# Kernel optimization log

Measured on AMD Instinct MI355X. Metric: run time of the kernel, lower is better.

Reference implementation:

```python
import jax, jax.numpy as jnp
import numpy as np

S, B, L, D, H, NOP = 4, 8, 512, 128, 128, 64  # segments, batch, seg_len, input_dim, hidden, n_operators
W = S * L  # 2048 total words
FT = 0.1   # forget-gate floor


def _norm_mat(m):
    # divide each row by its count of nonzero entries (torch normalize_matrix)
    cnt = (m != 0).sum(-1, keepdims=True).astype(m.dtype)
    return m / (cnt + 1e-30)


def _l2(x):
    return x / (jnp.linalg.norm(x, axis=-1, keepdims=True) + 1e-30)


def setup_inputs() -> dict:
    key = jax.random.key(0)
    ks = jax.random.split(key, 16)
    word_outputs = jax.random.normal(ks[0], (S, B, L, D), jnp.float32)
    node_hidden = jax.random.normal(ks[1], (B, D), jnp.float32)
    op_embedding = jax.random.normal(ks[2], (B, NOP, D), jnp.float32)
    word_operator = (jax.random.uniform(ks[3], (B, W, NOP)) < 0.05).astype(jnp.float32)
    word_word = (jax.random.uniform(ks[4], (B, W, W)) < 0.02).astype(jnp.float32)
    depend_relation = (jax.random.uniform(ks[5], (S, B, L, L)) < 0.05).astype(jnp.float32)
    word_exist_matrix = (jax.random.uniform(ks[6], (B, W, W)) < 0.9).astype(jnp.float32)
    word_exist_sequence = (jax.random.uniform(ks[7], (B, W)) < 0.9).astype(jnp.float32)
    goal_word = (jax.random.uniform(ks[8], (B, W)) < 0.2).astype(jnp.float32)

    def lin(k, fi, fo):
        k1, k2 = jax.random.split(k)
        s = 1.0 / np.sqrt(fi).astype(np.float32)
        return (jax.random.uniform(k1, (fi, fo), jnp.float32, -s, s),
                jax.random.uniform(k2, (fo,), jnp.float32, -s, s))

    o_w_W, o_w_b = lin(ks[9], D, H)
    wk_W, wk_b = lin(ks[10], D, H)
    ws_W, ws_b = lin(ks[11], D, H)
    up_W, up_b = lin(ks[12], 3 * H, D)
    wg_W, wg_b = lin(ks[13], D, D)
    fg_W, fg_b = lin(ks[14], 2 * D, D)
    return dict(word_outputs=word_outputs, node_hidden=node_hidden, op_embedding=op_embedding,
                word_operator=word_operator, word_word=word_word, depend_relation=depend_relation,
                word_exist_matrix=word_exist_matrix, word_exist_sequence=word_exist_sequence,
                goal_word=goal_word, o_w_W=o_w_W, o_w_b=o_w_b, wk_W=wk_W, wk_b=wk_b,
                ws_W=ws_W, ws_b=ws_b, up_W=up_W, up_b=up_b, wg_W=wg_W, wg_b=wg_b,
                fg_W=fg_W, fg_b=fg_b)


def reference(word_outputs, node_hidden, op_embedding, word_operator, word_word,
              depend_relation, word_exist_matrix, word_exist_sequence, goal_word,
              o_w_W, o_w_b, wk_W, wk_b, ws_W, ws_b, up_W, up_b, wg_W, wg_b, fg_W, fg_b):
    # cat(word_outputs, dim=1) -> [B, W, D]
    all_word = word_outputs.transpose(1, 0, 2, 3).reshape(B, W, D)
    # operator aggregation: [B,W,NOP] @ o_w(op_embedding) -> [B,W,H], L2-normalized
    word_o = _l2(jnp.einsum('bwo,boh->bwh', word_operator, op_embedding @ o_w_W + o_w_b))
    # knowledge aggregation over masked word-word adjacency
    adj_k = _norm_mat(word_word * word_exist_matrix)
    word_w_k = _l2(jnp.einsum('bvw,bwh->bvh', adj_k, all_word @ wk_W + wk_b))
    # per-segment dependency aggregation, then concat along word dim
    seg = jnp.einsum('sbij,sbjh->sbih', _norm_mat(depend_relation), word_outputs @ ws_W + ws_b)
    word_w_s = _l2(seg.transpose(1, 0, 2, 3).reshape(B, W, H))
    neighbor = jnp.concatenate([word_o, word_w_k, word_w_s], axis=-1)  # [B, W, 3H]
    word_updated = jax.nn.relu(neighbor @ up_W + up_b)  # [B, W, D]
    # goal pooling: bmm([B,1,W],[B,W,D]) -> [B,D]
    gw = _norm_mat(goal_word * word_exist_sequence)
    goal_w = jnp.einsum('bw,bwd->bd', gw, word_updated)
    goal_updated = jax.nn.relu(goal_w @ wg_W + wg_b)
    forget = jax.nn.sigmoid(jnp.concatenate([goal_w, node_hidden], axis=-1) @ fg_W + fg_b)
    return jnp.maximum(forget, FT) * node_hidden + (1.0 - forget) * goal_updated
```

## Files before the change

kernel.cpp:

```cpp
#include <hip/hip_runtime.h>
#include <math.h>

#define Sn 4
#define Bn 8
#define Ln 512
#define Dn 128
#define Hn 128
#define NOPn 64
#define Wn 2048


__device__ __forceinline__ float bf2f(unsigned short u) {
    return __uint_as_float(((unsigned int)u) << 16);
}
__device__ __forceinline__ float bflo(unsigned int u) {
    return __uint_as_float(u << 16);
}
__device__ __forceinline__ float bfhi(unsigned int u) {
    return __uint_as_float(u & 0xFFFF0000u);
}
__device__ __forceinline__ unsigned short f2bf(float f) {
    unsigned int u = __float_as_uint(f);
    return (unsigned short)((u + 0x7FFFu + ((u >> 16) & 1u)) >> 16);
}

typedef __attribute__((ext_vector_type(8))) short bf16x8;
typedef __attribute__((ext_vector_type(4))) float f32x4;

__global__ __launch_bounds__(256) void prep_k(const float* __restrict__ A,
                                              const float* __restrict__ W1,
                                              const float* __restrict__ W2,
                                              const float* __restrict__ b1,
                                              const float* __restrict__ b2,
                                              unsigned short* __restrict__ C1,
                                              unsigned short* __restrict__ C2,
                                              const float* __restrict__ ope,
                                              const float* __restrict__ owW,
                                              const float* __restrict__ owb,
                                              unsigned short* __restrict__ oph,
                                              const float* __restrict__ goal,
                                              const float* __restrict__ wes,
                                              int* __restrict__ widx,
                                              int* __restrict__ wcnt,
                                              float* __restrict__ gwacc,
                                              const float* __restrict__ upW,
                                              unsigned short* __restrict__ upWbf) {
    __shared__ __align__(16) unsigned char smem[33792];
    const int bid = blockIdx.x, tid = threadIdx.x;

    if (bid < 264) {
        unsigned short (*WT)[132] = reinterpret_cast<unsigned short(*)[132]>(smem);
        const bool dual = bid < 256;
        const int m0 = dual ? bid * 64 : (bid - 256) * 64;
        const float* Asrc = dual ? A : ope;
        const int lane = tid & 63, wr = tid >> 6;
        const int rloc = lane & 15, bsel = lane >> 4;

        bf16x8 af[4];
        const float* Arow = Asrc + (size_t)(m0 + wr * 16 + rloc) * 128;
#pragma unroll
        for (int ks = 0; ks < 4; ++ks) {
            float4 a0 = *reinterpret_cast<const float4*>(Arow + ks * 32 + 4 * bsel);
            float4 a1 = *reinterpret_cast<const float4*>(Arow + ks * 32 + 16 + 4 * bsel);
            af[ks][0] = (short)f2bf(a0.x); af[ks][1] = (short)f2bf(a0.y);
            af[ks][2] = (short)f2bf(a0.z); af[ks][3] = (short)f2bf(a0.w);
            af[ks][4] = (short)f2bf(a1.x); af[ks][5] = (short)f2bf(a1.y);
            af[ks][6] = (short)f2bf(a1.z); af[ks][7] = (short)f2bf(a1.w);
        }

        const int nmat = dual ? 2 : 1;
        for (int mat = 0; mat < nmat; ++mat) {
            const float* Wsrc = dual ? (mat ? W2 : W1) : owW;
            const float* bias = dual ? (mat ? b2 : b1) : owb;
            unsigned short* Cdst = dual ? (mat ? C2 : C1) : oph;
            __syncthreads();
            for (int idx = tid * 4; idx < 128 * 128; idx += 1024) {
                const int k = idx >> 7, c = idx & 127;
                float4 v = *reinterpret_cast<const float4*>(Wsrc + (size_t)k * 128 + c);
                WT[c + 0][k] = f2bf(v.x);
                WT[c + 1][k] = f2bf(v.y);
                WT[c + 2][k] = f2bf(v.z);
                WT[c + 3][k] = f2bf(v.w);
            }
            __syncthreads();

            f32x4 acc[8];
#pragma unroll
            for (int tl = 0; tl < 8; ++tl) acc[tl] = (f32x4){0.f, 0.f, 0.f, 0.f};
#pragma unroll
            for (int ks = 0; ks < 4; ++ks) {
#pragma unroll
                for (int tl = 0; tl < 8; ++tl) {
                    const unsigned short* p = &WT[tl * 16 + rloc][ks * 32 + 4 * bsel];
                    bf16x8 bfv;
#pragma unroll
                    for (int j = 0; j < 4; ++j) {
                        bfv[j]     = (short)p[j];
                        bfv[4 + j] = (short)p[16 + j];
                    }
                    acc[tl] = __builtin_amdgcn_mfma_f32_16x16x32_bf16(
                        af[ks], bfv, acc[tl], 0, 0, 0);
                }
            }
#pragma unroll
            for (int tl = 0; tl < 8; ++tl) {
                const int col = tl * 16 + rloc;
                const float bv = bias[col];
#pragma unroll
                for (int q = 0; q < 4; ++q) {
                    const int row = m0 + wr * 16 + bsel * 4 + q;
                    Cdst[(size_t)row * 128 + col] = f2bf(acc[tl][q] + bv);
                }
            }
        }
    } else if (bid < 272) {
        int* cnt = reinterpret_cast<int*>(smem);
        const int b = bid - 264;
        if (tid == 0) *cnt = 0;
        __syncthreads();
#pragma unroll
        for (int j = 0; j < 8; ++j) {
            const int w = tid * 8 + j;
            if (goal[b * Wn + w] != 0.f && wes[b * Wn + w] != 0.f) {
                const int p = atomicAdd(cnt, 1);
                if (p < 512) widx[b * 512 + p] = w;
            }
        }
        __syncthreads();
        if (tid == 0) wcnt[b] = *cnt < 512 ? *cnt : 512;
    } else if (bid == 272) {
        for (int idx = tid; idx < 1024; idx += 256) gwacc[idx] = 0.f;
    } else {
        const int base = (bid - 273) * 24576;
        for (int e = base + tid * 4; e < base + 24576; e += 1024) {
            float4 v = *reinterpret_cast<const float4*>(upW + e);
            alignas(8) unsigned short u[4] = {f2bf(v.x), f2bf(v.y), f2bf(v.z), f2bf(v.w)};
            *reinterpret_cast<uint2*>(upWbf + e) = *reinterpret_cast<const uint2*>(u);
        }
    }
}

__global__ __launch_bounds__(256) void mega_agg11(const int* __restrict__ widx,
                                                  const int* __restrict__ wcnt,
                                                  const float* __restrict__ ww,
                                                  const float* __restrict__ wem,
                                                  const float* __restrict__ dep,
                                                  const float* __restrict__ wop,
                                                  const unsigned short* __restrict__ oph,
                                                  const unsigned short* __restrict__ wkh,
                                                  const unsigned short* __restrict__ wsh,
                                                  const unsigned short* __restrict__ upWbf,
                                                  const float* __restrict__ upb,
                                                  float* __restrict__ gwacc) {
    const int bid = blockIdx.x;
    const int b = bid & 7, i = bid >> 3;
    if (i >= wcnt[b]) return;
    const int w_dst = widx[b * 512 + i];
    const int t = threadIdx.x;
    const int lane = t & 63, wv = t >> 6;

    __shared__ int kidx[512];
    __shared__ int sidx[256];
    __shared__ int kn, sn;
    __shared__ float part1[4][128];
    __shared__ float part2[4][128];
    __shared__ float nbL[384];
    __shared__ float gp16[16][128];
    if (t == 0) { kn = 0; sn = 0; }
    __syncthreads();

    const float* wwr = ww  + ((size_t)(b * Wn + w_dst)) * Wn;
    const float* wmr = wem + ((size_t)(b * Wn + w_dst)) * Wn;
#pragma unroll
    for (int q = 0; q < 2; ++q) {
        const int e0 = q * 1024 + t * 4;
        float4 v = *reinterpret_cast<const float4*>(wwr + e0);
        float4 m = *reinterpret_cast<const float4*>(wmr + e0);
        float vv[4] = {v.x, v.y, v.z, v.w};
        float mm[4] = {m.x, m.y, m.z, m.w};
#pragma unroll
        for (int j = 0; j < 4; ++j)
            if (vv[j] != 0.f && mm[j] != 0.f) {
                int p = atomicAdd(&kn, 1);
                if (p < 512) kidx[p] = e0 + j;
            }
    }
    const int sD = w_dst >> 9, lD = w_dst & 511;
    if (t < 128) {
        const float* dr = dep + ((size_t)((sD * Bn + b) * Ln + lD)) * Ln + t * 4;
        float4 v = *reinterpret_cast<const float4*>(dr);
        float vv[4] = {v.x, v.y, v.z, v.w};
#pragma unroll
        for (int j = 0; j < 4; ++j)
            if (vv[j] != 0.f) {
                int p = atomicAdd(&sn, 1);
                if (p < 256) sidx[p] = t * 4 + j;
            }
    }
    float m_op = 0.f;
    if (wv == 3) m_op = wop[((size_t)(b * Wn + w_dst)) * NOPn + lane];
    __syncthreads();

    const int nk = kn < 512 ? kn : 512;
    const int ns = sn < 256 ? sn : 256;
    const int ql = lane >> 4, c = lane & 15;

    {
        float a[8] = {};
        for (int p = wv * 4 + ql; p < nk; p += 16) {
            const int w = kidx[p];
            const int s = w >> 9, l = w & 511;
            const uint4 x = *reinterpret_cast<const uint4*>(
                wkh + ((size_t)((s * Bn + b) * Ln + l)) * Hn + c * 8);
            a[0] += bflo(x.x); a[1] += bfhi(x.x);
            a[2] += bflo(x.y); a[3] += bfhi(x.y);
            a[4] += bflo(x.z); a[5] += bfhi(x.z);
            a[6] += bflo(x.w); a[7] += bfhi(x.w);
        }
#pragma unroll
        for (int q = 0; q < 8; ++q) {
            a[q] += __shfl_xor(a[q], 16);
            a[q] += __shfl_xor(a[q], 32);
        }
        if (ql == 0) {
#pragma unroll
            for (int q = 0; q < 8; ++q) part1[wv][c * 8 + q] = a[q];
        }
    }
    {
        const unsigned short* base = wsh + (size_t)((sD * Bn + b) * Ln) * Hn + c * 8;
        float a[8] = {};
        for (int p = wv * 4 + ql; p < ns; p += 16) {
            const uint4 x = *reinterpret_cast<const uint4*>(base + (size_t)sidx[p] * Hn);
            a[0] += bflo(x.x); a[1] += bfhi(x.x);
            a[2] += bflo(x.y); a[3] += bfhi(x.y);
            a[4] += bflo(x.z); a[5] += bfhi(x.z);
            a[6] += bflo(x.w); a[7] += bfhi(x.w);
        }
#pragma unroll
        for (int q = 0; q < 8; ++q) {
            a[q] += __shfl_xor(a[q], 16);
            a[q] += __shfl_xor(a[q], 32);
        }
        if (ql == 0) {
#pragma unroll
            for (int q = 0; q < 8; ++q) part2[wv][c * 8 + q] = a[q];
        }
    }
    if (wv == 3) {
        unsigned long long bal = __ballot(m_op != 0.f);
        float a0 = 0.f, a1 = 0.f;
        const unsigned short* base = oph + (size_t)b * NOPn * Hn + 2 * lane;
        while (bal) {
            const int o = __ffsll(bal) - 1;
            bal &= bal - 1;
            ushort2 v = *reinterpret_cast<const ushort2*>(base + o * Hn);
            a0 += bf2f(v.x);
            a1 += bf2f(v.y);
        }
        float ss = a0 * a0 + a1 * a1;
#pragma unroll
        for (int off = 1; off < 64; off <<= 1) ss += __shfl_xor(ss, off);
        const float sc = 1.f / (sqrtf(ss) + 1e-30f);
        nbL[2 * lane]     = a0 * sc;
        nbL[2 * lane + 1] = a1 * sc;
    }
    __syncthreads();

    if (wv == 0) {
        float s0 = 0.f, s1 = 0.f;
#pragma unroll
        for (int q = 0; q < 4; ++q) {
            s0 += part1[q][2 * lane];
            s1 += part1[q][2 * lane + 1];
        }
        float ss = s0 * s0 + s1 * s1;
#pragma unroll
        for (int off = 1; off < 64; off <<= 1) ss += __shfl_xor(ss, off);
        const float sc = 1.f / (sqrtf(ss) + 1e-30f);
        nbL[128 + 2 * lane]     = s0 * sc;
        nbL[128 + 2 * lane + 1] = s1 * sc;
    } else if (wv == 1) {
        float s0 = 0.f, s1 = 0.f;
#pragma unroll
        for (int q = 0; q < 4; ++q) {
            s0 += part2[q][2 * lane];
            s1 += part2[q][2 * lane + 1];
        }
        float ss = s0 * s0 + s1 * s1;
#pragma unroll
        for (int off = 1; off < 64; off <<= 1) ss += __shfl_xor(ss, off);
        const float sc = 1.f / (sqrtf(ss) + 1e-30f);
        nbL[256 + 2 * lane]     = s0 * sc;
        nbL[256 + 2 * lane + 1] = s1 * sc;
    }
    __syncthreads();

    {
        const int i8 = (t & 15) * 8, j = t >> 4;
        float a[8] = {};
#pragma unroll
        for (int r = 0; r < 24; ++r) {
            const int k = r * 16 + j;
            const uint4 w = *reinterpret_cast<const uint4*>(upWbf + (size_t)k * 128 + i8);
            const float x = nbL[k];
            a[0] = fmaf(x, bflo(w.x), a[0]); a[1] = fmaf(x, bfhi(w.x), a[1]);
            a[2] = fmaf(x, bflo(w.y), a[2]); a[3] = fmaf(x, bfhi(w.y), a[3]);
            a[4] = fmaf(x, bflo(w.z), a[4]); a[5] = fmaf(x, bfhi(w.z), a[5]);
            a[6] = fmaf(x, bflo(w.w), a[6]); a[7] = fmaf(x, bfhi(w.w), a[7]);
        }
#pragma unroll
        for (int q = 0; q < 8; ++q) gp16[j][i8 + q] = a[q];
    }
    __syncthreads();
    if (t < 128) {
        float g = upb[t];
#pragma unroll
        for (int j = 0; j < 16; ++j) g += gp16[j][t];
        g = fmaxf(g, 0.f);
        atomicAdd(&gwacc[b * 128 + t], g);
    }
}

__global__ __launch_bounds__(128) void final4_k(const int* __restrict__ wcnt,
                                                const float* __restrict__ gwacc,
                                                const float* __restrict__ nh,
                                                const float* __restrict__ wgW,
                                                const float* __restrict__ wgb,
                                                const float* __restrict__ fgW,
                                                const float* __restrict__ fgb,
                                                float* __restrict__ out) {
    const int b = blockIdx.x, t = threadIdx.x;
    __shared__ float gw[Dn], nhs[Dn];
    const float inv = 1.f / ((float)wcnt[b] + 1e-30f);
    gw[t]  = gwacc[b * Dn + t] * inv;
    nhs[t] = nh[b * Dn + t];
    __syncthreads();
    float gu = wgb[t];
    for (int d = 0; d < Dn; ++d) gu = fmaf(gw[d], wgW[d * Dn + t], gu);
    gu = fmaxf(gu, 0.f);
    float fg = fgb[t];
    for (int d = 0; d < Dn; ++d) fg = fmaf(gw[d], fgW[d * Dn + t], fg);
    for (int d = 0; d < Dn; ++d) fg = fmaf(nhs[d], fgW[(Dn + d) * Dn + t], fg);
    const float forget = 1.f / (1.f + expf(-fg));
    out[b * Dn + t] = fmaxf(forget, 0.1f) * nhs[t] + (1.f - forget) * gu;
}

extern "C" void kernel_launch(void* const* d_in, const int* in_sizes, int n_in,
                              void* d_out, int out_size, void* d_ws, size_t ws_size,
                              hipStream_t stream) {
    (void)in_sizes; (void)n_in; (void)out_size; (void)ws_size;
    const float* word_outputs        = (const float*)d_in[0];
    const float* node_hidden         = (const float*)d_in[1];
    const float* op_embedding        = (const float*)d_in[2];
    const float* word_operator       = (const float*)d_in[3];
    const float* word_word           = (const float*)d_in[4];
    const float* depend_relation     = (const float*)d_in[5];
    const float* word_exist_matrix   = (const float*)d_in[6];
    const float* word_exist_sequence = (const float*)d_in[7];
    const float* goal_word           = (const float*)d_in[8];
    const float* o_w_W = (const float*)d_in[9];
    const float* o_w_b = (const float*)d_in[10];
    const float* wk_W  = (const float*)d_in[11];
    const float* wk_b  = (const float*)d_in[12];
    const float* ws_W  = (const float*)d_in[13];
    const float* ws_b  = (const float*)d_in[14];
    const float* up_W  = (const float*)d_in[15];
    const float* up_b  = (const float*)d_in[16];
    const float* wg_W  = (const float*)d_in[17];
    const float* wg_b  = (const float*)d_in[18];
    const float* fg_W  = (const float*)d_in[19];
    const float* fg_b  = (const float*)d_in[20];
    float* out = (float*)d_out;

    char* ws = (char*)d_ws;
    unsigned short* oph   = (unsigned short*)(ws + 0);
    unsigned short* wkh   = (unsigned short*)(ws + (1u << 20));
    unsigned short* wsh   = (unsigned short*)(ws + (5u << 20));
    int* widx             = (int*)(ws + (9u << 20));
    int* wcnt             = (int*)(ws + (9u << 20) + 32768);
    float* gwacc          = (float*)(ws + (9u << 20) + 65536);
    unsigned short* upWbf = (unsigned short*)(ws + (9u << 20) + 131072);

    prep_k<<<275, 256, 0, stream>>>(word_outputs, wk_W, ws_W, wk_b, ws_b, wkh, wsh,
                                    op_embedding, o_w_W, o_w_b, oph,
                                    goal_word, word_exist_sequence, widx, wcnt, gwacc,
                                    up_W, upWbf);
    mega_agg11<<<4096, 256, 0, stream>>>(widx, wcnt, word_word, word_exist_matrix,
                                         depend_relation, word_operator, oph, wkh, wsh,
                                         upWbf, up_b, gwacc);
    final4_k<<<8, 128, 0, stream>>>(wcnt, gwacc, node_hidden,
                                    wg_W, wg_b, fg_W, fg_b, out);
}
```

Before: 334.8 us.

## Move sparse index list construction from aggregation kernel into prep kernel

```diff
diff --git a/kernel.cpp b/kernel.cpp
--- a/kernel.cpp
+++ b/kernel.cpp
@@ -44,7 +44,14 @@
                                               int* __restrict__ wcnt,
                                               float* __restrict__ gwacc,
                                               const float* __restrict__ upW,
-                                              unsigned short* __restrict__ upWbf) {
+                                              unsigned short* __restrict__ upWbf,
+                                              const float* __restrict__ ww,
+                                              const float* __restrict__ wem,
+                                              const float* __restrict__ dep,
+                                              int* __restrict__ klist,
+                                              int* __restrict__ kcnt,
+                                              int* __restrict__ slist,
+                                              int* __restrict__ scnt) {
     __shared__ __align__(16) unsigned char smem[33792];
     const int bid = blockIdx.x, tid = threadIdx.x;
 
@@ -130,21 +137,74 @@
         if (tid == 0) wcnt[b] = *cnt < 512 ? *cnt : 512;
     } else if (bid == 272) {
         for (int idx = tid; idx < 1024; idx += 256) gwacc[idx] = 0.f;
-    } else {
+    } else if (bid < 275) {
         const int base = (bid - 273) * 24576;
         for (int e = base + tid * 4; e < base + 24576; e += 1024) {
             float4 v = *reinterpret_cast<const float4*>(upW + e);
             alignas(8) unsigned short u[4] = {f2bf(v.x), f2bf(v.y), f2bf(v.z), f2bf(v.w)};
             *reinterpret_cast<uint2*>(upWbf + e) = *reinterpret_cast<const uint2*>(u);
         }
-    }
-}
-
-__global__ __launch_bounds__(256) void mega_agg11(const int* __restrict__ widx,
+    } else {
+        int* list = reinterpret_cast<int*>(smem);
+        int* cnt  = reinterpret_cast<int*>(smem + 2048);
+        const int rbase = (bid - 275) * 8;
+        for (int jr = 0; jr < 8; ++jr) {
+            const int r = rbase + jr;
+            const int b = r >> 11, w = r & 2047;
+            if (goal[b * Wn + w] == 0.f || wes[b * Wn + w] == 0.f) continue;
+            if (tid == 0) *cnt = 0;
+            __syncthreads();
+            const float* wwr = ww  + (size_t)r * Wn;
+            const float* wmr = wem + (size_t)r * Wn;
+#pragma unroll
+            for (int q = 0; q < 2; ++q) {
+                const int e0 = q * 1024 + tid * 4;
+                float4 v = *reinterpret_cast<const float4*>(wwr + e0);
+                float4 m = *reinterpret_cast<const float4*>(wmr + e0);
+                float vv[4] = {v.x, v.y, v.z, v.w};
+                float mm[4] = {m.x, m.y, m.z, m.w};
+#pragma unroll
+                for (int j = 0; j < 4; ++j)
+                    if (vv[j] != 0.f && mm[j] != 0.f) {
+                        const int p = atomicAdd(cnt, 1);
+                        if (p < 512) list[p] = e0 + j;
+                    }
+            }
+            __syncthreads();
+            const int nk = *cnt < 512 ? *cnt : 512;
+            if (tid == 0) kcnt[r] = nk;
+            for (int p = tid; p < nk; p += 256) klist[(size_t)r * 512 + p] = list[p];
+            __syncthreads();
+            if (tid == 0) *cnt = 0;
+            __syncthreads();
+            const int sD = w >> 9, lD = w & 511;
+            const float* dr = dep + ((size_t)((sD * Bn + b) * Ln + lD)) * Ln;
+            {
+                const int e0 = tid * 2;
+                float2 v = *reinterpret_cast<const float2*>(dr + e0);
+                float vv[2] = {v.x, v.y};
+#pragma unroll
+                for (int j = 0; j < 2; ++j)
+                    if (vv[j] != 0.f) {
+                        const int p = atomicAdd(cnt, 1);
+                        if (p < 256) list[p] = e0 + j;
+                    }
+            }
+            __syncthreads();
+            const int ns = *cnt < 256 ? *cnt : 256;
+            if (tid == 0) scnt[r] = ns;
+            for (int p = tid; p < ns; p += 256) slist[(size_t)r * 256 + p] = list[p];
+            __syncthreads();
+        }
+    }
+}
+
+__global__ __launch_bounds__(256) void mega_agg12(const int* __restrict__ widx,
                                                   const int* __restrict__ wcnt,
-                                                  const float* __restrict__ ww,
-                                                  const float* __restrict__ wem,
-                                                  const float* __restrict__ dep,
+                                                  const int* __restrict__ klist,
+                                                  const int* __restrict__ kcnt,
+                                                  const int* __restrict__ slist,
+                                                  const int* __restrict__ scnt,
                                                   const float* __restrict__ wop,
                                                   const unsigned short* __restrict__ oph,
                                                   const unsigned short* __restrict__ wkh,
@@ -159,56 +219,23 @@
     const int t = threadIdx.x;
     const int lane = t & 63, wv = t >> 6;
 
-    __shared__ int kidx[512];
-    __shared__ int sidx[256];
-    __shared__ int kn, sn;
     __shared__ float part1[4][128];
     __shared__ float part2[4][128];
     __shared__ float nbL[384];
     __shared__ float gp16[16][128];
-    if (t == 0) { kn = 0; sn = 0; }
-    __syncthreads();
-
-    const float* wwr = ww  + ((size_t)(b * Wn + w_dst)) * Wn;
-    const float* wmr = wem + ((size_t)(b * Wn + w_dst)) * Wn;
-#pragma unroll
-    for (int q = 0; q < 2; ++q) {
-        const int e0 = q * 1024 + t * 4;
-        float4 v = *reinterpret_cast<const float4*>(wwr + e0);
-        float4 m = *reinterpret_cast<const float4*>(wmr + e0);
-        float vv[4] = {v.x, v.y, v.z, v.w};
-        float mm[4] = {m.x, m.y, m.z, m.w};
-#pragma unroll
-        for (int j = 0; j < 4; ++j)
-            if (vv[j] != 0.f && mm[j] != 0.f) {
-                int p = atomicAdd(&kn, 1);
-                if (p < 512) kidx[p] = e0 + j;
-            }
-    }
-    const int sD = w_dst >> 9, lD = w_dst & 511;
-    if (t < 128) {
-        const float* dr = dep + ((size_t)((sD * Bn + b) * Ln + lD)) * Ln + t * 4;
-        float4 v = *reinterpret_cast<const float4*>(dr);
-        float vv[4] = {v.x, v.y, v.z, v.w};
-#pragma unroll
-        for (int j = 0; j < 4; ++j)
-            if (vv[j] != 0.f) {
-                int p = atomicAdd(&sn, 1);
-                if (p < 256) sidx[p] = t * 4 + j;
-            }
-    }
-    float m_op = 0.f;
-    if (wv == 3) m_op = wop[((size_t)(b * Wn + w_dst)) * NOPn + lane];
-    __syncthreads();
-
-    const int nk = kn < 512 ? kn : 512;
-    const int ns = sn < 256 ? sn : 256;
+
+    const int r = b * Wn + w_dst;
+    const int sD = w_dst >> 9;
+    const int nk = kcnt[r];
+    const int ns = scnt[r];
     const int ql = lane >> 4, c = lane & 15;
+    const int* krow = klist + (size_t)r * 512;
+    const int* srow = slist + (size_t)r * 256;
 
     {
         float a[8] = {};
         for (int p = wv * 4 + ql; p < nk; p += 16) {
-            const int w = kidx[p];
+            const int w = krow[p];
             const int s = w >> 9, l = w & 511;
             const uint4 x = *reinterpret_cast<const uint4*>(
                 wkh + ((size_t)((s * Bn + b) * Ln + l)) * Hn + c * 8);
@@ -231,7 +258,7 @@
         const unsigned short* base = wsh + (size_t)((sD * Bn + b) * Ln) * Hn + c * 8;
         float a[8] = {};
         for (int p = wv * 4 + ql; p < ns; p += 16) {
-            const uint4 x = *reinterpret_cast<const uint4*>(base + (size_t)sidx[p] * Hn);
+            const uint4 x = *reinterpret_cast<const uint4*>(base + (size_t)srow[p] * Hn);
             a[0] += bflo(x.x); a[1] += bfhi(x.x);
             a[2] += bflo(x.y); a[3] += bfhi(x.y);
             a[4] += bflo(x.z); a[5] += bfhi(x.z);
@@ -248,6 +275,7 @@
         }
     }
     if (wv == 3) {
+        const float m_op = wop[((size_t)r) * NOPn + lane];
         unsigned long long bal = __ballot(m_op != 0.f);
         float a0 = 0.f, a1 = 0.f;
         const unsigned short* base = oph + (size_t)b * NOPn * Hn + 2 * lane;
@@ -300,8 +328,8 @@
         const int i8 = (t & 15) * 8, j = t >> 4;
         float a[8] = {};
 #pragma unroll
-        for (int r = 0; r < 24; ++r) {
-            const int k = r * 16 + j;
+        for (int rr = 0; rr < 24; ++rr) {
+            const int k = rr * 16 + j;
             const uint4 w = *reinterpret_cast<const uint4*>(upWbf + (size_t)k * 128 + i8);
             const float x = nbL[k];
             a[0] = fmaf(x, bflo(w.x), a[0]); a[1] = fmaf(x, bfhi(w.x), a[1]);
@@ -381,13 +409,19 @@
     int* wcnt             = (int*)(ws + (9u << 20) + 32768);
     float* gwacc          = (float*)(ws + (9u << 20) + 65536);
     unsigned short* upWbf = (unsigned short*)(ws + (9u << 20) + 131072);
-
-    prep_k<<<275, 256, 0, stream>>>(word_outputs, wk_W, ws_W, wk_b, ws_b, wkh, wsh,
-                                    op_embedding, o_w_W, o_w_b, oph,
-                                    goal_word, word_exist_sequence, widx, wcnt, gwacc,
-                                    up_W, upWbf);
-    mega_agg11<<<4096, 256, 0, stream>>>(widx, wcnt, word_word, word_exist_matrix,
-                                         depend_relation, word_operator, oph, wkh, wsh,
+    int* klist            = (int*)(ws + (16u << 20));
+    int* kcnt             = (int*)(ws + (48u << 20));
+    int* slist            = (int*)(ws + (49u << 20));
+    int* scnt             = (int*)(ws + (66u << 20));
+
+    prep_k<<<2323, 256, 0, stream>>>(word_outputs, wk_W, ws_W, wk_b, ws_b, wkh, wsh,
+                                     op_embedding, o_w_W, o_w_b, oph,
+                                     goal_word, word_exist_sequence, widx, wcnt, gwacc,
+                                     up_W, upWbf,
+                                     word_word, word_exist_matrix, depend_relation,
+                                     klist, kcnt, slist, scnt);
+    mega_agg12<<<4096, 256, 0, stream>>>(widx, wcnt, klist, kcnt, slist, scnt,
+                                         word_operator, oph, wkh, wsh,
                                          upWbf, up_b, gwacc);
     final4_k<<<8, 128, 0, stream>>>(wcnt, gwacc, node_hidden,
                                     wg_W, wg_b, fg_W, fg_b, out);
```

Result: no change. 337.3 us (+0.7%).
